# Optimization experiments

Hardware: AMD Instinct MI355X
Metric: run time of the kernel (lower is better)

## Reference

```python
import jax, jax.numpy as jnp
import numpy as np

B, T, C_EMB, C_HEAD = 4, 4096, 1024, 64

def setup_inputs() -> dict:
    key = jax.random.key(0)
    kx, kk, kq, kv = jax.random.split(key, 4)
    x = jax.random.normal(kx, (B, T, C_EMB), dtype=jnp.float32)
    # nn.Linear(C_EMB, C_HEAD, bias=False); store as (in, out) so projection is x @ W
    Wk = jax.random.normal(kk, (C_EMB, C_HEAD), dtype=jnp.float32) * 0.02
    Wq = jax.random.normal(kq, (C_EMB, C_HEAD), dtype=jnp.float32) * 0.02
    Wv = jax.random.normal(kv, (C_EMB, C_HEAD), dtype=jnp.float32) * 0.02
    return {"x": x, "Wk": Wk, "Wq": Wq, "Wv": Wv}

def reference(x, Wk, Wq, Wv):
    k = x @ Wk  # [B,T,Ch]
    q = x @ Wq
    v = x @ Wv
    scale = C_HEAD ** -0.5
    weights = jnp.einsum('bqc,bkc->bqk', q, k) * scale  # [B,T,T]
    causal = jnp.tril(jnp.ones((T, T), dtype=bool))
    weights = jnp.where(causal, weights, -jnp.inf)
    # NOTE: original uses F.softmax(dim=1), i.e. over the QUERY (row) axis -> axis=-2
    weights = jax.nn.softmax(weights, axis=-2)
    # dropout_rate=0.0 (eval) -> identity
    return jnp.einsum('bqk,bkc->bqc', weights, v)
```

## Files before the change

### kernel.cpp

```cpp
#include <hip/hip_runtime.h>
#include <math.h>

#define BB 4
#define TT 4096
#define CE 1024
#define CH 64
#define SCALE2 0.18033688011112042f
#define NQT 64
#define NZ 4

typedef unsigned short ushort_t;
typedef __attribute__((ext_vector_type(8))) short bf16x8;
typedef __attribute__((ext_vector_type(8))) unsigned short u16x8;
typedef __attribute__((ext_vector_type(4))) float f32x4;

__device__ __forceinline__ unsigned short f2bf(float f) {
    unsigned int x = __builtin_bit_cast(unsigned int, f);
    unsigned int r = x + 0x7fffu + ((x >> 16) & 1u);
    return (unsigned short)(r >> 16);
}
__device__ __forceinline__ float bf2f(unsigned short u) {
    unsigned int x = ((unsigned int)u) << 16;
    return __builtin_bit_cast(float, x);
}

__device__ __forceinline__ void stage_tile(const ushort_t* __restrict__ src,
                                           ushort_t (*dst)[68], int tg)
{
#pragma unroll
    for (int i = 0; i < 2; ++i) {
        const int idx = i * 256 + tg;
        const int row = idx >> 3, c0 = (idx & 7) * 8;
        u16x8 v = *(const u16x8*)(src + (long)idx * 8);
        union { u16x8 v; uint2 q[2]; } uu; uu.v = v;
        *(uint2*)&dst[row][c0]     = uu.q[0];
        *(uint2*)&dst[row][c0 + 4] = uu.q[1];
    }
}

__device__ __forceinline__ void stage_tile512(const ushort_t* __restrict__ src,
                                              ushort_t (*dst)[68], int tid)
{
    const int row = tid >> 3, c0 = (tid & 7) * 8;
    u16x8 v = *(const u16x8*)(src + (long)tid * 8);
    union { u16x8 v; uint2 q[2]; } uu; uu.v = v;
    *(uint2*)&dst[row][c0]     = uu.q[0];
    *(uint2*)&dst[row][c0 + 4] = uu.q[1];
}

__device__ __forceinline__ bf16x8 frag68(const ushort_t* p) {
    union { bf16x8 v; uint2 q[2]; } uu;
    uu.q[0] = *(const uint2*)p;
    uu.q[1] = *(const uint2*)(p + 4);
    return uu.v;
}

__global__ __launch_bounds__(256)
void wt_build(const float* __restrict__ Wk, const float* __restrict__ Wq,
              const float* __restrict__ Wv, ushort_t* __restrict__ wt2)
{
    const int m = blockIdx.x, kt = blockIdx.y;
    const float* __restrict__ W = (m == 0) ? Wk : (m == 1 ? Wq : Wv);
    const int k0 = kt * 64;
    __shared__ float lds[64][65];
    const int cc = threadIdx.x & 63, g = threadIdx.x >> 6;
#pragma unroll
    for (int i = 0; i < 16; ++i) {
        const int r = g * 16 + i;
        lds[r][cc] = W[(k0 + r) * CH + cc];
    }
    __syncthreads();
    const int k = k0 + cc;
#pragma unroll
    for (int i = 0; i < 16; ++i) {
        const int c = g * 16 + i;
        wt2[((long)(k >> 5) * 192 + (m * 64 + c)) * 32 + (k & 31)] = f2bf(lds[cc][c]);
    }
}

__global__ __launch_bounds__(512)
void proj_mfma(const float* __restrict__ x, const ushort_t* __restrict__ wt2,
               ushort_t* __restrict__ qb, ushort_t* __restrict__ kb, ushort_t* __restrict__ vb)
{
    const int tid = threadIdx.x;
    const int w = tid >> 6, l = tid & 63, lg = l >> 4, lr = l & 15;
    const int wr = w >> 2, wc = w & 3;
    const long t0 = (long)blockIdx.x * 32;

    __shared__ ushort_t As[32][68];
    __shared__ ushort_t Bs[192][68];

    f32x4 acc[3];
#pragma unroll
    for (int nf = 0; nf < 3; ++nf) acc[nf] = (f32x4){0.f, 0.f, 0.f, 0.f};

    const int arow = tid >> 4, acol = (tid & 15) * 4;
    const float* __restrict__ xsrc = x + (t0 + arow) * CE + acol;

    int bc[3], bh[3], bk[3];
#pragma unroll
    for (int i = 0; i < 3; ++i) {
        const int idx = i * 512 + tid;
        const int h = idx >= 768;
        const int j = idx - h * 768;
        bc[i] = j >> 2; bh[i] = h; bk[i] = (j & 3) * 8;
    }

    float4 a4 = *(const float4*)(xsrc);
    u16x8 bv[3];
#pragma unroll
    for (int i = 0; i < 3; ++i)
        bv[i] = *(const u16x8*)(wt2 + ((long)(bh[i]) * 192 + bc[i]) * 32 + bk[i]);

    for (int step = 0; step < 16; ++step) {
        {
            uint2 pk;
            pk.x = (unsigned)f2bf(a4.x) | ((unsigned)f2bf(a4.y) << 16);
            pk.y = (unsigned)f2bf(a4.z) | ((unsigned)f2bf(a4.w) << 16);
            *(uint2*)&As[arow][acol] = pk;
#pragma unroll
            for (int i = 0; i < 3; ++i) {
                union { u16x8 v; uint2 q[2]; } uu; uu.v = bv[i];
                ushort_t* d = &Bs[bc[i]][bh[i] * 32 + bk[i]];
                *(uint2*)d = uu.q[0];
                *(uint2*)(d + 4) = uu.q[1];
            }
        }
        __syncthreads();
        if (step < 15) {
            const int k0n = (step + 1) * 64;
            a4 = *(const float4*)(xsrc + k0n);
            const int ktn = k0n >> 5;
#pragma unroll
            for (int i = 0; i < 3; ++i)
                bv[i] = *(const u16x8*)(wt2 + ((long)(ktn + bh[i]) * 192 + bc[i]) * 32 + bk[i]);
        }
#pragma unroll
        for (int h = 0; h < 2; ++h) {
            bf16x8 af = frag68(&As[wr * 16 + lr][h * 32 + lg * 8]);
#pragma unroll
            for (int nf = 0; nf < 3; ++nf) {
                bf16x8 bf = frag68(&Bs[wc * 48 + nf * 16 + lr][h * 32 + lg * 8]);
                acc[nf] = __builtin_amdgcn_mfma_f32_16x16x32_bf16(af, bf, acc[nf], 0, 0, 0);
            }
        }
        __syncthreads();
    }

    ushort_t* Os = &Bs[0][0];
#pragma unroll
    for (int nf = 0; nf < 3; ++nf)
#pragma unroll
        for (int r = 0; r < 4; ++r)
            Os[(wr * 16 + lg * 4 + r) * 200 + wc * 48 + nf * 16 + lr] = f2bf(acc[nf][r]);
    __syncthreads();
    if (tid < 256) {
        const int row = tid >> 3, c0 = (tid & 7) * 8;
#pragma unroll
        for (int m = 0; m < 3; ++m) {
            u16x8 ov = *(const u16x8*)&Os[row * 200 + m * 64 + c0];
            ushort_t* __restrict__ outp = (m == 0) ? kb : (m == 1 ? qb : vb);
            *(u16x8*)(outp + (t0 + row) * CH + c0) = ov;
        }
    }
}

__global__ __launch_bounds__(512)
void colstats_mfma(const ushort_t* __restrict__ qb, const ushort_t* __restrict__ kb,
                   float* __restrict__ pl)
{
    const int b = blockIdx.x, p = blockIdx.y, z = blockIdx.z;
    const int tid = threadIdx.x;
    const int w = tid >> 6, l = tid & 63, lg = l >> 4, lr = l & 15;
    const int wg = w >> 2, wc = w & 3, tg = tid & 255;
    const long baseT = (long)b * TT;
    const long NTT = (long)BB * TT;

    __shared__ ushort_t Ks[64][68], Qs[2][64][68];
    __shared__ float redc[4][64][5];

    for (int pass = 0; pass < 2; ++pass) {
        const int kt = pass ? (63 - p) : p;
        stage_tile512(kb + (baseT + (long)kt * 64) * CH, Ks, tid);
        __syncthreads();
        bf16x8 ka0 = frag68(&Ks[wc * 16 + lr][lg * 8]);
        bf16x8 ka1 = frag68(&Ks[wc * 16 + lr][32 + lg * 8]);

        float l_r[4] = {0.f, 0.f, 0.f, 0.f};

        const int j0 = kt + ((z - kt) & (NZ - 1));
        const int n0 = (j0 < NQT) ? ((NQT - 1 - j0) >> 3) + 1 : 0;
        for (int i = 0; i < n0; ++i) {
            const int j = j0 + 4 * wg + 8 * i;
            const bool act = (j < NQT);
            if (act) stage_tile(qb + (baseT + (long)j * 64) * CH, Qs[wg], tg);
            __syncthreads();
            if (act) {
                const bool diag = (j == kt);
#pragma unroll
                for (int qf = 0; qf < 4; ++qf) {
                    bf16x8 b0 = frag68(&Qs[wg][qf * 16 + lr][lg * 8]);
                    bf16x8 b1 = frag68(&Qs[wg][qf * 16 + lr][32 + lg * 8]);
                    f32x4 s = {0.f, 0.f, 0.f, 0.f};
                    s = __builtin_amdgcn_mfma_f32_16x16x32_bf16(ka0, b0, s, 0, 0, 0);
                    s = __builtin_amdgcn_mfma_f32_16x16x32_bf16(ka1, b1, s, 0, 0, 0);
#pragma unroll
                    for (int r = 0; r < 4; ++r) {
                        float ev = exp2f(s[r] * SCALE2);
                        if (diag && (qf * 16 + lr) < (wc * 16 + lg * 4 + r)) ev = 0.f;
                        l_r[r] += ev;
                    }
                }
            }
            __syncthreads();
        }
        if (wg == 1) {
#pragma unroll
            for (int r = 0; r < 4; ++r) redc[wc][l][r] = l_r[r];
        }
        __syncthreads();
        if (wg == 0) {
#pragma unroll
            for (int r = 0; r < 4; ++r) {
                float lv = l_r[r] + redc[wc][l][r];
                for (int d = 1; d < 16; d <<= 1) lv += __shfl_xor(lv, d);
                if (lr == 0) {
                    const long k = (long)kt * 64 + wc * 16 + lg * 4 + r;
                    pl[(long)z * NTT + baseT + k] = lv;
                }
            }
        }
        __syncthreads();
    }
}

__global__ __launch_bounds__(256)
void vt_scale(const ushort_t* __restrict__ vb, const float* __restrict__ pl,
              ushort_t* __restrict__ vtb2)
{
    const int b = blockIdx.x;
    const int jt = blockIdx.y;
    const long t0 = (long)jt * 64;
    const int tid = threadIdx.x;
    __shared__ ushort_t lds[64][72];
    const long baseT = (long)b * TT;
    const long NTT = (long)BB * TT;
#pragma unroll
    for (int i = 0; i < 2; ++i) {
        const int t = i * 32 + (tid >> 3);
        const int c0 = (tid & 7) * 8;
        u16x8 v = *(const u16x8*)(vb + (baseT + t0 + t) * CH + c0);
        const long idx = baseT + t0 + t;
        float ls = pl[idx];
#pragma unroll
        for (int zz = 1; zz < NZ; ++zz) ls += pl[zz * NTT + idx];
        const float sc = 1.f / ls;
#pragma unroll
        for (int j = 0; j < 8; ++j) lds[c0 + j][t] = f2bf(bf2f(v[j]) * sc);
    }
    __syncthreads();
    ushort_t* __restrict__ dst = vtb2 + ((long)(b * 64 + jt)) * (64 * 64);
#pragma unroll
    for (int i = 0; i < 2; ++i) {
        const int c = i * 32 + (tid >> 3);
        const int tt0 = (tid & 7) * 8;
        u16x8 ov = *(const u16x8*)&lds[c][tt0];
        *(u16x8*)(dst + (long)c * 64 + tt0) = ov;
    }
}

__global__ __launch_bounds__(512)
void pv_mfma(const ushort_t* __restrict__ qb, const ushort_t* __restrict__ kb,
             const ushort_t* __restrict__ vtb2, float* __restrict__ pout)
{
    const int b = blockIdx.x, p = blockIdx.y, z = blockIdx.z;
    const int tid = threadIdx.x;
    const int w = tid >> 6, l = tid & 63, lg = l >> 4, lr = l & 15;
    const int wg = w >> 2, wc = w & 3, tg = tid & 255;
    const long baseT = (long)b * TT;
    const long NTT = (long)BB * TT;

    __shared__ ushort_t Qs[64][68], Ks[2][64][68], Vs[2][64][68], Ps[2][64][68];
    __shared__ float redp[4][64][17];

    for (int pass = 0; pass < 2; ++pass) {
        const int qt = pass ? (63 - p) : p;
        stage_tile512(qb + (baseT + (long)qt * 64) * CH, Qs, tid);
        __syncthreads();
        bf16x8 qf_[4][2];
#pragma unroll
        for (int qf = 0; qf < 4; ++qf) {
            qf_[qf][0] = frag68(&Qs[qf * 16 + lr][lg * 8]);
            qf_[qf][1] = frag68(&Qs[qf * 16 + lr][32 + lg * 8]);
        }
        f32x4 o[4];
#pragma unroll
        for (int qf = 0; qf < 4; ++qf) o[qf] = (f32x4){0.f, 0.f, 0.f, 0.f};

        const int n0 = (qt >= z) ? ((qt - z) >> 3) + 1 : 0;
        for (int i = 0; i < n0; ++i) {
            const int j = z + 4 * wg + 8 * i;
            const bool act = (j <= qt);
            if (act) {
                stage_tile(kb + (baseT + (long)j * 64) * CH, Ks[wg], tg);
                stage_tile(vtb2 + ((long)(b * 64 + j)) * (64 * 64), Vs[wg], tg);
            }
            __syncthreads();
            bf16x8 va0, va1;
            if (act) {
                bf16x8 ka0 = frag68(&Ks[wg][wc * 16 + lr][lg * 8]);
                bf16x8 ka1 = frag68(&Ks[wg][wc * 16 + lr][32 + lg * 8]);
                va0 = frag68(&Vs[wg][wc * 16 + lr][lg * 8]);
                va1 = frag68(&Vs[wg][wc * 16 + lr][32 + lg * 8]);
                const bool diag = (j == qt);
#pragma unroll
                for (int qf = 0; qf < 4; ++qf) {
                    f32x4 s = {0.f, 0.f, 0.f, 0.f};
                    s = __builtin_amdgcn_mfma_f32_16x16x32_bf16(ka0, qf_[qf][0], s, 0, 0, 0);
                    s = __builtin_amdgcn_mfma_f32_16x16x32_bf16(ka1, qf_[qf][1], s, 0, 0, 0);
                    unsigned short e[4];
#pragma unroll
                    for (int r = 0; r < 4; ++r) {
                        float ev = exp2f(s[r] * SCALE2);
                        if (diag && (qf * 16 + lr) < (wc * 16 + lg * 4 + r)) ev = 0.f;
                        e[r] = f2bf(ev);
                    }
                    uint2 pk;
                    pk.x = (unsigned)e[0] | ((unsigned)e[1] << 16);
                    pk.y = (unsigned)e[2] | ((unsigned)e[3] << 16);
                    *(uint2*)&Ps[wg][qf * 16 + lr][wc * 16 + lg * 4] = pk;
                }
            }
            __syncthreads();
            if (act) {
#pragma unroll
                for (int qf = 0; qf < 4; ++qf) {
                    bf16x8 p0 = frag68(&Ps[wg][qf * 16 + lr][lg * 8]);
                    bf16x8 p1 = frag68(&Ps[wg][qf * 16 + lr][32 + lg * 8]);
                    o[qf] = __builtin_amdgcn_mfma_f32_16x16x32_bf16(va0, p0, o[qf], 0, 0, 0);
                    o[qf] = __builtin_amdgcn_mfma_f32_16x16x32_bf16(va1, p1, o[qf], 0, 0, 0);
                }
            }
        }
        if (wg == 1) {
#pragma unroll
            for (int qf = 0; qf < 4; ++qf)
#pragma unroll
                for (int r = 0; r < 4; ++r) redp[wc][l][qf * 4 + r] = o[qf][r];
        }
        __syncthreads();
        if (wg == 0) {
            float* pz = pout + ((long)z * NTT + baseT + (long)qt * 64) * CH;
#pragma unroll
            for (int qf = 0; qf < 4; ++qf) {
                f32x4 ov = o[qf];
#pragma unroll
                for (int r = 0; r < 4; ++r) ov[r] += redp[wc][l][qf * 4 + r];
                *(f32x4*)(pz + (long)(qf * 16 + lr) * CH + wc * 16 + lg * 4) = ov;
            }
        }
        __syncthreads();
    }
}

__global__ __launch_bounds__(256)
void finalize_out(const float* __restrict__ pout, float* __restrict__ out)
{
    const long i = (long)blockIdx.x * 256 + threadIdx.x;
    const long n4 = (long)BB * TT * CH / 4;
    float4 r = reinterpret_cast<const float4*>(pout)[i];
#pragma unroll
    for (int zz = 1; zz < NZ; ++zz) {
        float4 a = reinterpret_cast<const float4*>(pout)[zz * n4 + i];
        r.x += a.x; r.y += a.y; r.z += a.z; r.w += a.w;
    }
    reinterpret_cast<float4*>(out)[i] = r;
}

extern "C" void kernel_launch(void* const* d_in, const int* in_sizes, int n_in,
                              void* d_out, int out_size, void* d_ws, size_t ws_size,
                              hipStream_t stream)
{
    const float* x  = (const float*)d_in[0];
    const float* Wk = (const float*)d_in[1];
    const float* Wq = (const float*)d_in[2];
    const float* Wv = (const float*)d_in[3];
    float* out = (float*)d_out;

    const size_t NT = (size_t)BB * TT;
    ushort_t* qb   = (ushort_t*)d_ws;
    ushort_t* kb   = qb + NT * CH;
    ushort_t* vb   = kb + NT * CH;
    ushort_t* vtb2 = vb + NT * CH;
    ushort_t* wt2  = vtb2 + NT * CH;
    float* pl   = (float*)(wt2 + 192 * CE);
    float* pout = pl + NZ * NT;

    hipLaunchKernelGGL(wt_build, dim3(3, 16), dim3(256), 0, stream,
                       Wk, Wq, Wv, wt2);
    hipLaunchKernelGGL(proj_mfma, dim3(NT / 32), dim3(512), 0, stream,
                       x, wt2, qb, kb, vb);
    hipLaunchKernelGGL(colstats_mfma, dim3(BB, NQT / 2, NZ), dim3(512), 0, stream,
                       qb, kb, pl);
    hipLaunchKernelGGL(vt_scale, dim3(BB, TT / 64), dim3(256), 0, stream,
                       vb, pl, vtb2);
    hipLaunchKernelGGL(pv_mfma, dim3(BB, NQT / 2, NZ), dim3(512), 0, stream,
                       qb, kb, vtb2, pout);
    hipLaunchKernelGGL(finalize_out, dim3(NT * CH / 4 / 256), dim3(256), 0, stream,
                       pout, out);
}
```

Measured before the change: 75.89 us.

## Prefetch Q/K/V tiles into registers and fold column normalisation into PV

The colstats and pv kernels now load the next tile into registers while the current tile is computed, a software prefetch that hides global-load latency behind the MFMA work. The projection kernel writes V directly in the transposed tile layout. The vt_scale pass is replaced by a small kernel that computes per-key inverse column sums, and that scale is applied to the exponentials inside pv_mfma. This removes one read and one write of V, at the cost of extra registers and a per-tile float4 load of the inverse sums.

```diff
diff --git a/kernel.cpp b/kernel.cpp
--- a/kernel.cpp
+++ b/kernel.cpp
@@ -24,20 +24,22 @@
     return __builtin_bit_cast(float, x);
 }
 
-__device__ __forceinline__ void stage_tile(const ushort_t* __restrict__ src,
-                                           ushort_t (*dst)[68], int tg)
+__device__ __forceinline__ void tile_load2(const ushort_t* __restrict__ src, int tg, u16x8* r)
+{
+    r[0] = *(const u16x8*)(src + (long)tg * 8);
+    r[1] = *(const u16x8*)(src + (long)(256 + tg) * 8);
+}
+__device__ __forceinline__ void tile_store2(ushort_t (*dst)[68], int tg, const u16x8* r)
 {
 #pragma unroll
     for (int i = 0; i < 2; ++i) {
         const int idx = i * 256 + tg;
         const int row = idx >> 3, c0 = (idx & 7) * 8;
-        u16x8 v = *(const u16x8*)(src + (long)idx * 8);
-        union { u16x8 v; uint2 q[2]; } uu; uu.v = v;
+        union { u16x8 v; uint2 q[2]; } uu; uu.v = r[i];
         *(uint2*)&dst[row][c0]     = uu.q[0];
         *(uint2*)&dst[row][c0 + 4] = uu.q[1];
     }
 }
-
 __device__ __forceinline__ void stage_tile512(const ushort_t* __restrict__ src,
                                               ushort_t (*dst)[68], int tid)
 {
@@ -80,7 +82,7 @@
 
 __global__ __launch_bounds__(512)
 void proj_mfma(const float* __restrict__ x, const ushort_t* __restrict__ wt2,
-               ushort_t* __restrict__ qb, ushort_t* __restrict__ kb, ushort_t* __restrict__ vb)
+               ushort_t* __restrict__ qb, ushort_t* __restrict__ kb, ushort_t* __restrict__ vtb2)
 {
     const int tid = threadIdx.x;
     const int w = tid >> 6, l = tid & 63, lg = l >> 4, lr = l & 15;
@@ -157,11 +159,17 @@
     if (tid < 256) {
         const int row = tid >> 3, c0 = (tid & 7) * 8;
 #pragma unroll
-        for (int m = 0; m < 3; ++m) {
+        for (int m = 0; m < 2; ++m) {
             u16x8 ov = *(const u16x8*)&Os[row * 200 + m * 64 + c0];
-            ushort_t* __restrict__ outp = (m == 0) ? kb : (m == 1 ? qb : vb);
+            ushort_t* __restrict__ outp = (m == 0) ? kb : qb;
             *(u16x8*)(outp + (t0 + row) * CH + c0) = ov;
         }
+        const int c = tid >> 2, ii = tid & 3;
+        u16x8 tv;
+#pragma unroll
+        for (int k = 0; k < 8; ++k) tv[k] = Os[(ii * 8 + k) * 200 + 128 + c];
+        const int bI = (int)(t0 / TT), jt = (int)((t0 % TT) >> 6), toff = (int)(t0 & 63);
+        *(u16x8*)(vtb2 + (((long)(bI * 64 + jt) * 64 + c) * 64) + toff + ii * 8) = tv;
     }
 }
 
@@ -182,19 +190,27 @@
     for (int pass = 0; pass < 2; ++pass) {
         const int kt = pass ? (63 - p) : p;
         stage_tile512(kb + (baseT + (long)kt * 64) * CH, Ks, tid);
+
+        float l_r[4] = {0.f, 0.f, 0.f, 0.f};
+        const int j0 = kt + ((z - kt) & (NZ - 1));
+        const int n0 = (j0 < NQT) ? ((NQT - 1 - j0) >> 3) + 1 : 0;
+
+        u16x8 qreg[2];
+        {
+            const int j = j0 + 4 * wg;
+            if (j < NQT) tile_load2(qb + (baseT + (long)j * 64) * CH, tg, qreg);
+        }
         __syncthreads();
         bf16x8 ka0 = frag68(&Ks[wc * 16 + lr][lg * 8]);
         bf16x8 ka1 = frag68(&Ks[wc * 16 + lr][32 + lg * 8]);
 
-        float l_r[4] = {0.f, 0.f, 0.f, 0.f};
-
-        const int j0 = kt + ((z - kt) & (NZ - 1));
-        const int n0 = (j0 < NQT) ? ((NQT - 1 - j0) >> 3) + 1 : 0;
         for (int i = 0; i < n0; ++i) {
             const int j = j0 + 4 * wg + 8 * i;
             const bool act = (j < NQT);
-            if (act) stage_tile(qb + (baseT + (long)j * 64) * CH, Qs[wg], tg);
+            if (act) tile_store2(Qs[wg], tg, qreg);
             __syncthreads();
+            const int jn = j + 8;
+            if (jn < NQT) tile_load2(qb + (baseT + (long)jn * 64) * CH, tg, qreg);
             if (act) {
                 const bool diag = (j == kt);
 #pragma unroll
@@ -235,43 +251,20 @@
 }
 
 __global__ __launch_bounds__(256)
-void vt_scale(const ushort_t* __restrict__ vb, const float* __restrict__ pl,
-              ushort_t* __restrict__ vtb2)
-{
-    const int b = blockIdx.x;
-    const int jt = blockIdx.y;
-    const long t0 = (long)jt * 64;
-    const int tid = threadIdx.x;
-    __shared__ ushort_t lds[64][72];
-    const long baseT = (long)b * TT;
+void linv_kernel(const float* __restrict__ pl, float* __restrict__ linv)
+{
+    const long i = (long)blockIdx.x * 256 + threadIdx.x;
     const long NTT = (long)BB * TT;
-#pragma unroll
-    for (int i = 0; i < 2; ++i) {
-        const int t = i * 32 + (tid >> 3);
-        const int c0 = (tid & 7) * 8;
-        u16x8 v = *(const u16x8*)(vb + (baseT + t0 + t) * CH + c0);
-        const long idx = baseT + t0 + t;
-        float ls = pl[idx];
-#pragma unroll
-        for (int zz = 1; zz < NZ; ++zz) ls += pl[zz * NTT + idx];
-        const float sc = 1.f / ls;
-#pragma unroll
-        for (int j = 0; j < 8; ++j) lds[c0 + j][t] = f2bf(bf2f(v[j]) * sc);
-    }
-    __syncthreads();
-    ushort_t* __restrict__ dst = vtb2 + ((long)(b * 64 + jt)) * (64 * 64);
-#pragma unroll
-    for (int i = 0; i < 2; ++i) {
-        const int c = i * 32 + (tid >> 3);
-        const int tt0 = (tid & 7) * 8;
-        u16x8 ov = *(const u16x8*)&lds[c][tt0];
-        *(u16x8*)(dst + (long)c * 64 + tt0) = ov;
-    }
+    float s = pl[i];
+#pragma unroll
+    for (int zz = 1; zz < NZ; ++zz) s += pl[zz * NTT + i];
+    linv[i] = 1.f / s;
 }
 
 __global__ __launch_bounds__(512)
 void pv_mfma(const ushort_t* __restrict__ qb, const ushort_t* __restrict__ kb,
-             const ushort_t* __restrict__ vtb2, float* __restrict__ pout)
+             const ushort_t* __restrict__ vtb2, const float* __restrict__ linv,
+             float* __restrict__ pout)
 {
     const int b = blockIdx.x, p = blockIdx.y, z = blockIdx.z;
     const int tid = threadIdx.x;
@@ -286,6 +279,16 @@
     for (int pass = 0; pass < 2; ++pass) {
         const int qt = pass ? (63 - p) : p;
         stage_tile512(qb + (baseT + (long)qt * 64) * CH, Qs, tid);
+
+        const int n0 = (qt >= z) ? ((qt - z) >> 3) + 1 : 0;
+        u16x8 kreg[2], vreg[2];
+        {
+            const int j = z + 4 * wg;
+            if (j <= qt) {
+                tile_load2(kb + (baseT + (long)j * 64) * CH, tg, kreg);
+                tile_load2(vtb2 + ((long)(b * 64 + j)) * 4096, tg, vreg);
+            }
+        }
         __syncthreads();
         bf16x8 qf_[4][2];
 #pragma unroll
@@ -297,21 +300,27 @@
 #pragma unroll
         for (int qf = 0; qf < 4; ++qf) o[qf] = (f32x4){0.f, 0.f, 0.f, 0.f};
 
-        const int n0 = (qt >= z) ? ((qt - z) >> 3) + 1 : 0;
         for (int i = 0; i < n0; ++i) {
             const int j = z + 4 * wg + 8 * i;
             const bool act = (j <= qt);
             if (act) {
-                stage_tile(kb + (baseT + (long)j * 64) * CH, Ks[wg], tg);
-                stage_tile(vtb2 + ((long)(b * 64 + j)) * (64 * 64), Vs[wg], tg);
+                tile_store2(Ks[wg], tg, kreg);
+                tile_store2(Vs[wg], tg, vreg);
             }
             __syncthreads();
+            const int jn = j + 8;
+            if (jn <= qt) {
+                tile_load2(kb + (baseT + (long)jn * 64) * CH, tg, kreg);
+                tile_load2(vtb2 + ((long)(b * 64 + jn)) * 4096, tg, vreg);
+            }
             bf16x8 va0, va1;
             if (act) {
                 bf16x8 ka0 = frag68(&Ks[wg][wc * 16 + lr][lg * 8]);
                 bf16x8 ka1 = frag68(&Ks[wg][wc * 16 + lr][32 + lg * 8]);
                 va0 = frag68(&Vs[wg][wc * 16 + lr][lg * 8]);
                 va1 = frag68(&Vs[wg][wc * 16 + lr][32 + lg * 8]);
+                float4 lv4 = *(const float4*)(linv + baseT + (long)j * 64 + wc * 16 + lg * 4);
+                const float lvr[4] = {lv4.x, lv4.y, lv4.z, lv4.w};
                 const bool diag = (j == qt);
 #pragma unroll
                 for (int qf = 0; qf < 4; ++qf) {
@@ -321,7 +330,7 @@
                     unsigned short e[4];
 #pragma unroll
                     for (int r = 0; r < 4; ++r) {
-                        float ev = exp2f(s[r] * SCALE2);
+                        float ev = exp2f(s[r] * SCALE2) * lvr[r];
                         if (diag && (qf * 16 + lr) < (wc * 16 + lg * 4 + r)) ev = 0.f;
                         e[r] = f2bf(ev);
                     }
@@ -390,22 +399,22 @@
     const size_t NT = (size_t)BB * TT;
     ushort_t* qb   = (ushort_t*)d_ws;
     ushort_t* kb   = qb + NT * CH;
-    ushort_t* vb   = kb + NT * CH;
-    ushort_t* vtb2 = vb + NT * CH;
+    ushort_t* vtb2 = kb + NT * CH;
     ushort_t* wt2  = vtb2 + NT * CH;
     float* pl   = (float*)(wt2 + 192 * CE);
-    float* pout = pl + NZ * NT;
+    float* linv = pl + NZ * NT;
+    float* pout = linv + NT;
 
     hipLaunchKernelGGL(wt_build, dim3(3, 16), dim3(256), 0, stream,
                        Wk, Wq, Wv, wt2);
     hipLaunchKernelGGL(proj_mfma, dim3(NT / 32), dim3(512), 0, stream,
-                       x, wt2, qb, kb, vb);
+                       x, wt2, qb, kb, vtb2);
     hipLaunchKernelGGL(colstats_mfma, dim3(BB, NQT / 2, NZ), dim3(512), 0, stream,
                        qb, kb, pl);
-    hipLaunchKernelGGL(vt_scale, dim3(BB, TT / 64), dim3(256), 0, stream,
-                       vb, pl, vtb2);
+    hipLaunchKernelGGL(linv_kernel, dim3(NT / 256), dim3(256), 0, stream,
+                       pl, linv);
     hipLaunchKernelGGL(pv_mfma, dim3(BB, NQT / 2, NZ), dim3(512), 0, stream,
-                       qb, kb, vtb2, pout);
+                       qb, kb, vtb2, linv, pout);
     hipLaunchKernelGGL(finalize_out, dim3(NT * CH / 4 / 256), dim3(256), 0, stream,
                        pout, out);
 }
```

New measurement: 83.20 us. +9.6%, slower.

## Prefetch tiles into registers and launch one tile per block in attention kernels

Applied to the files above, without the earlier changes.

Both colstats and pv kernels now load the next Q (or K/V) tile into registers while the current tile is being computed, then write it to LDS at the top of the next iteration. This hides global-memory latency behind MFMA work. The paired two-pass scheme per block is dropped in favour of one tile per block with twice as many blocks, and pv_mfma reverses tile order so the heaviest tiles are scheduled first. LDS use is reduced by aliasing the reduction buffer onto Ks and reusing Qs as one wave group's P buffer, which may raise occupancy but also raises register pressure.

```diff
diff --git a/kernel.cpp b/kernel.cpp
--- a/kernel.cpp
+++ b/kernel.cpp
@@ -24,20 +24,22 @@
     return __builtin_bit_cast(float, x);
 }
 
-__device__ __forceinline__ void stage_tile(const ushort_t* __restrict__ src,
-                                           ushort_t (*dst)[68], int tg)
+__device__ __forceinline__ void tile_load2(const ushort_t* __restrict__ src, int tg, u16x8* r)
+{
+    r[0] = *(const u16x8*)(src + (long)tg * 8);
+    r[1] = *(const u16x8*)(src + (long)(256 + tg) * 8);
+}
+__device__ __forceinline__ void tile_store2(ushort_t (*dst)[68], int tg, const u16x8* r)
 {
 #pragma unroll
     for (int i = 0; i < 2; ++i) {
         const int idx = i * 256 + tg;
         const int row = idx >> 3, c0 = (idx & 7) * 8;
-        u16x8 v = *(const u16x8*)(src + (long)idx * 8);
-        union { u16x8 v; uint2 q[2]; } uu; uu.v = v;
+        union { u16x8 v; uint2 q[2]; } uu; uu.v = r[i];
         *(uint2*)&dst[row][c0]     = uu.q[0];
         *(uint2*)&dst[row][c0 + 4] = uu.q[1];
     }
 }
-
 __device__ __forceinline__ void stage_tile512(const ushort_t* __restrict__ src,
                                               ushort_t (*dst)[68], int tid)
 {
@@ -169,7 +171,7 @@
 void colstats_mfma(const ushort_t* __restrict__ qb, const ushort_t* __restrict__ kb,
                    float* __restrict__ pl)
 {
-    const int b = blockIdx.x, p = blockIdx.y, z = blockIdx.z;
+    const int b = blockIdx.x, kt = blockIdx.y, z = blockIdx.z;
     const int tid = threadIdx.x;
     const int w = tid >> 6, l = tid & 63, lg = l >> 4, lr = l & 15;
     const int wg = w >> 2, wc = w & 3, tg = tid & 255;
@@ -179,58 +181,62 @@
     __shared__ ushort_t Ks[64][68], Qs[2][64][68];
     __shared__ float redc[4][64][5];
 
-    for (int pass = 0; pass < 2; ++pass) {
-        const int kt = pass ? (63 - p) : p;
-        stage_tile512(kb + (baseT + (long)kt * 64) * CH, Ks, tid);
-        __syncthreads();
-        bf16x8 ka0 = frag68(&Ks[wc * 16 + lr][lg * 8]);
-        bf16x8 ka1 = frag68(&Ks[wc * 16 + lr][32 + lg * 8]);
-
-        float l_r[4] = {0.f, 0.f, 0.f, 0.f};
-
-        const int j0 = kt + ((z - kt) & (NZ - 1));
-        const int n0 = (j0 < NQT) ? ((NQT - 1 - j0) >> 3) + 1 : 0;
-        for (int i = 0; i < n0; ++i) {
-            const int j = j0 + 4 * wg + 8 * i;
-            const bool act = (j < NQT);
-            if (act) stage_tile(qb + (baseT + (long)j * 64) * CH, Qs[wg], tg);
-            __syncthreads();
-            if (act) {
-                const bool diag = (j == kt);
-#pragma unroll
-                for (int qf = 0; qf < 4; ++qf) {
-                    bf16x8 b0 = frag68(&Qs[wg][qf * 16 + lr][lg * 8]);
-                    bf16x8 b1 = frag68(&Qs[wg][qf * 16 + lr][32 + lg * 8]);
-                    f32x4 s = {0.f, 0.f, 0.f, 0.f};
-                    s = __builtin_amdgcn_mfma_f32_16x16x32_bf16(ka0, b0, s, 0, 0, 0);
-                    s = __builtin_amdgcn_mfma_f32_16x16x32_bf16(ka1, b1, s, 0, 0, 0);
-#pragma unroll
-                    for (int r = 0; r < 4; ++r) {
-                        float ev = exp2f(s[r] * SCALE2);
-                        if (diag && (qf * 16 + lr) < (wc * 16 + lg * 4 + r)) ev = 0.f;
-                        l_r[r] += ev;
-                    }
+    stage_tile512(kb + (baseT + (long)kt * 64) * CH, Ks, tid);
+
+    float l_r[4] = {0.f, 0.f, 0.f, 0.f};
+    const int j0 = kt + ((z - kt) & (NZ - 1));
+    const int n0 = (j0 < NQT) ? ((NQT - 1 - j0) >> 3) + 1 : 0;
+
+    u16x8 qreg[2];
+    {
+        const int j = j0 + 4 * wg;
+        if (j < NQT) tile_load2(qb + (baseT + (long)j * 64) * CH, tg, qreg);
+    }
+    __syncthreads();
+    bf16x8 ka0 = frag68(&Ks[wc * 16 + lr][lg * 8]);
+    bf16x8 ka1 = frag68(&Ks[wc * 16 + lr][32 + lg * 8]);
+
+    for (int i = 0; i < n0; ++i) {
+        const int j = j0 + 4 * wg + 8 * i;
+        const bool act = (j < NQT);
+        if (act) tile_store2(Qs[wg], tg, qreg);
+        __syncthreads();
+        const int jn = j + 8;
+        if (jn < NQT) tile_load2(qb + (baseT + (long)jn * 64) * CH, tg, qreg);
+        if (act) {
+            const bool diag = (j == kt);
+#pragma unroll
+            for (int qf = 0; qf < 4; ++qf) {
+                bf16x8 b0 = frag68(&Qs[wg][qf * 16 + lr][lg * 8]);
+                bf16x8 b1 = frag68(&Qs[wg][qf * 16 + lr][32 + lg * 8]);
+                f32x4 s = {0.f, 0.f, 0.f, 0.f};
+                s = __builtin_amdgcn_mfma_f32_16x16x32_bf16(ka0, b0, s, 0, 0, 0);
+                s = __builtin_amdgcn_mfma_f32_16x16x32_bf16(ka1, b1, s, 0, 0, 0);
+#pragma unroll
+                for (int r = 0; r < 4; ++r) {
+                    float ev = exp2f(s[r] * SCALE2);
+                    if (diag && (qf * 16 + lr) < (wc * 16 + lg * 4 + r)) ev = 0.f;
+                    l_r[r] += ev;
                 }
             }
-            __syncthreads();
-        }
-        if (wg == 1) {
-#pragma unroll
-            for (int r = 0; r < 4; ++r) redc[wc][l][r] = l_r[r];
-        }
-        __syncthreads();
-        if (wg == 0) {
-#pragma unroll
-            for (int r = 0; r < 4; ++r) {
-                float lv = l_r[r] + redc[wc][l][r];
-                for (int d = 1; d < 16; d <<= 1) lv += __shfl_xor(lv, d);
-                if (lr == 0) {
-                    const long k = (long)kt * 64 + wc * 16 + lg * 4 + r;
-                    pl[(long)z * NTT + baseT + k] = lv;
-                }
-            }
-        }
-        __syncthreads();
+        }
+        __syncthreads();
+    }
+    if (wg == 1) {
+#pragma unroll
+        for (int r = 0; r < 4; ++r) redc[wc][l][r] = l_r[r];
+    }
+    __syncthreads();
+    if (wg == 0) {
+#pragma unroll
+        for (int r = 0; r < 4; ++r) {
+            float lv = l_r[r] + redc[wc][l][r];
+            for (int d = 1; d < 16; d <<= 1) lv += __shfl_xor(lv, d);
+            if (lr == 0) {
+                const long k = (long)kt * 64 + wc * 16 + lg * 4 + r;
+                pl[(long)z * NTT + baseT + k] = lv;
+            }
+        }
     }
 }
 
@@ -273,93 +279,110 @@
 void pv_mfma(const ushort_t* __restrict__ qb, const ushort_t* __restrict__ kb,
              const ushort_t* __restrict__ vtb2, float* __restrict__ pout)
 {
-    const int b = blockIdx.x, p = blockIdx.y, z = blockIdx.z;
+    const int b = blockIdx.x, z = blockIdx.z;
+    const int qt = 63 - blockIdx.y;
     const int tid = threadIdx.x;
     const int w = tid >> 6, l = tid & 63, lg = l >> 4, lr = l & 15;
     const int wg = w >> 2, wc = w & 3, tg = tid & 255;
     const long baseT = (long)b * TT;
     const long NTT = (long)BB * TT;
 
-    __shared__ ushort_t Qs[64][68], Ks[2][64][68], Vs[2][64][68], Ps[2][64][68];
-    __shared__ float redp[4][64][17];
-
-    for (int pass = 0; pass < 2; ++pass) {
-        const int qt = pass ? (63 - p) : p;
-        stage_tile512(qb + (baseT + (long)qt * 64) * CH, Qs, tid);
-        __syncthreads();
-        bf16x8 qf_[4][2];
+    __shared__ ushort_t Qs[64][68];
+    __shared__ ushort_t Ks[2][64][68];
+    __shared__ ushort_t Vs[2][64][68];
+    __shared__ ushort_t Ps1[64][68];
+    float (*redp)[64][17] = (float (*)[64][17])&Ks[0][0][0];
+
+    stage_tile512(qb + (baseT + (long)qt * 64) * CH, Qs, tid);
+
+    const int n0 = (qt >= z) ? ((qt - z) >> 3) + 1 : 0;
+    u16x8 kreg[2], vreg[2];
+    {
+        const int j = z + 4 * wg;
+        if (j <= qt) {
+            tile_load2(kb + (baseT + (long)j * 64) * CH, tg, kreg);
+            tile_load2(vtb2 + ((long)(b * 64 + j)) * 4096, tg, vreg);
+        }
+    }
+    __syncthreads();
+    bf16x8 qf_[4][2];
+#pragma unroll
+    for (int qf = 0; qf < 4; ++qf) {
+        qf_[qf][0] = frag68(&Qs[qf * 16 + lr][lg * 8]);
+        qf_[qf][1] = frag68(&Qs[qf * 16 + lr][32 + lg * 8]);
+    }
+    f32x4 o[4];
+#pragma unroll
+    for (int qf = 0; qf < 4; ++qf) o[qf] = (f32x4){0.f, 0.f, 0.f, 0.f};
+
+    ushort_t (*Pbuf)[68] = (wg == 0) ? Qs : Ps1;
+
+    for (int i = 0; i < n0; ++i) {
+        const int j = z + 4 * wg + 8 * i;
+        const bool act = (j <= qt);
+        if (act) {
+            tile_store2(Ks[wg], tg, kreg);
+            tile_store2(Vs[wg], tg, vreg);
+        }
+        __syncthreads();
+        const int jn = j + 8;
+        if (jn <= qt) {
+            tile_load2(kb + (baseT + (long)jn * 64) * CH, tg, kreg);
+            tile_load2(vtb2 + ((long)(b * 64 + jn)) * 4096, tg, vreg);
+        }
+        bf16x8 va0, va1;
+        if (act) {
+            bf16x8 ka0 = frag68(&Ks[wg][wc * 16 + lr][lg * 8]);
+            bf16x8 ka1 = frag68(&Ks[wg][wc * 16 + lr][32 + lg * 8]);
+            va0 = frag68(&Vs[wg][wc * 16 + lr][lg * 8]);
+            va1 = frag68(&Vs[wg][wc * 16 + lr][32 + lg * 8]);
+            const bool diag = (j == qt);
+#pragma unroll
+            for (int qf = 0; qf < 4; ++qf) {
+                f32x4 s = {0.f, 0.f, 0.f, 0.f};
+                s = __builtin_amdgcn_mfma_f32_16x16x32_bf16(ka0, qf_[qf][0], s, 0, 0, 0);
+                s = __builtin_amdgcn_mfma_f32_16x16x32_bf16(ka1, qf_[qf][1], s, 0, 0, 0);
+                unsigned short e[4];
+#pragma unroll
+                for (int r = 0; r < 4; ++r) {
+                    float ev = exp2f(s[r] * SCALE2);
+                    if (diag && (qf * 16 + lr) < (wc * 16 + lg * 4 + r)) ev = 0.f;
+                    e[r] = f2bf(ev);
+                }
+                uint2 pk;
+                pk.x = (unsigned)e[0] | ((unsigned)e[1] << 16);
+                pk.y = (unsigned)e[2] | ((unsigned)e[3] << 16);
+                *(uint2*)&Pbuf[qf * 16 + lr][wc * 16 + lg * 4] = pk;
+            }
+        }
+        __syncthreads();
+        if (act) {
+#pragma unroll
+            for (int qf = 0; qf < 4; ++qf) {
+                bf16x8 p0 = frag68(&Pbuf[qf * 16 + lr][lg * 8]);
+                bf16x8 p1 = frag68(&Pbuf[qf * 16 + lr][32 + lg * 8]);
+                o[qf] = __builtin_amdgcn_mfma_f32_16x16x32_bf16(va0, p0, o[qf], 0, 0, 0);
+                o[qf] = __builtin_amdgcn_mfma_f32_16x16x32_bf16(va1, p1, o[qf], 0, 0, 0);
+            }
+        }
+        __syncthreads();
+    }
+    if (wg == 1) {
+#pragma unroll
+        for (int qf = 0; qf < 4; ++qf)
+#pragma unroll
+            for (int r = 0; r < 4; ++r) redp[wc][l][qf * 4 + r] = o[qf][r];
+    }
+    __syncthreads();
+    if (wg == 0) {
+        float* pz = pout + ((long)z * NTT + baseT + (long)qt * 64) * CH;
 #pragma unroll
         for (int qf = 0; qf < 4; ++qf) {
-            qf_[qf][0] = frag68(&Qs[qf * 16 + lr][lg * 8]);
-            qf_[qf][1] = frag68(&Qs[qf * 16 + lr][32 + lg * 8]);
-        }
-        f32x4 o[4];
-#pragma unroll
-        for (int qf = 0; qf < 4; ++qf) o[qf] = (f32x4){0.f, 0.f, 0.f, 0.f};
-
-        const int n0 = (qt >= z) ? ((qt - z) >> 3) + 1 : 0;
-        for (int i = 0; i < n0; ++i) {
-            const int j = z + 4 * wg + 8 * i;
-            const bool act = (j <= qt);
-            if (act) {
-                stage_tile(kb + (baseT + (long)j * 64) * CH, Ks[wg], tg);
-                stage_tile(vtb2 + ((long)(b * 64 + j)) * (64 * 64), Vs[wg], tg);
-            }
-            __syncthreads();
-            bf16x8 va0, va1;
-            if (act) {
-                bf16x8 ka0 = frag68(&Ks[wg][wc * 16 + lr][lg * 8]);
-                bf16x8 ka1 = frag68(&Ks[wg][wc * 16 + lr][32 + lg * 8]);
-                va0 = frag68(&Vs[wg][wc * 16 + lr][lg * 8]);
-                va1 = frag68(&Vs[wg][wc * 16 + lr][32 + lg * 8]);
-                const bool diag = (j == qt);
-#pragma unroll
-                for (int qf = 0; qf < 4; ++qf) {
-                    f32x4 s = {0.f, 0.f, 0.f, 0.f};
-                    s = __builtin_amdgcn_mfma_f32_16x16x32_bf16(ka0, qf_[qf][0], s, 0, 0, 0);
-                    s = __builtin_amdgcn_mfma_f32_16x16x32_bf16(ka1, qf_[qf][1], s, 0, 0, 0);
-                    unsigned short e[4];
-#pragma unroll
-                    for (int r = 0; r < 4; ++r) {
-                        float ev = exp2f(s[r] * SCALE2);
-                        if (diag && (qf * 16 + lr) < (wc * 16 + lg * 4 + r)) ev = 0.f;
-                        e[r] = f2bf(ev);
-                    }
-                    uint2 pk;
-                    pk.x = (unsigned)e[0] | ((unsigned)e[1] << 16);
-                    pk.y = (unsigned)e[2] | ((unsigned)e[3] << 16);
-                    *(uint2*)&Ps[wg][qf * 16 + lr][wc * 16 + lg * 4] = pk;
-                }
-            }
-            __syncthreads();
-            if (act) {
-#pragma unroll
-                for (int qf = 0; qf < 4; ++qf) {
-                    bf16x8 p0 = frag68(&Ps[wg][qf * 16 + lr][lg * 8]);
-                    bf16x8 p1 = frag68(&Ps[wg][qf * 16 + lr][32 + lg * 8]);
-                    o[qf] = __builtin_amdgcn_mfma_f32_16x16x32_bf16(va0, p0, o[qf], 0, 0, 0);
-                    o[qf] = __builtin_amdgcn_mfma_f32_16x16x32_bf16(va1, p1, o[qf], 0, 0, 0);
-                }
-            }
-        }
-        if (wg == 1) {
-#pragma unroll
-            for (int qf = 0; qf < 4; ++qf)
-#pragma unroll
-                for (int r = 0; r < 4; ++r) redp[wc][l][qf * 4 + r] = o[qf][r];
-        }
-        __syncthreads();
-        if (wg == 0) {
-            float* pz = pout + ((long)z * NTT + baseT + (long)qt * 64) * CH;
-#pragma unroll
-            for (int qf = 0; qf < 4; ++qf) {
-                f32x4 ov = o[qf];
-#pragma unroll
-                for (int r = 0; r < 4; ++r) ov[r] += redp[wc][l][qf * 4 + r];
-                *(f32x4*)(pz + (long)(qf * 16 + lr) * CH + wc * 16 + lg * 4) = ov;
-            }
-        }
-        __syncthreads();
+            f32x4 ov = o[qf];
+#pragma unroll
+            for (int r = 0; r < 4; ++r) ov[r] += redp[wc][l][qf * 4 + r];
+            *(f32x4*)(pz + (long)(qf * 16 + lr) * CH + wc * 16 + lg * 4) = ov;
+        }
     }
 }
 
@@ -400,11 +423,11 @@
                        Wk, Wq, Wv, wt2);
     hipLaunchKernelGGL(proj_mfma, dim3(NT / 32), dim3(512), 0, stream,
                        x, wt2, qb, kb, vb);
-    hipLaunchKernelGGL(colstats_mfma, dim3(BB, NQT / 2, NZ), dim3(512), 0, stream,
+    hipLaunchKernelGGL(colstats_mfma, dim3(BB, NQT, NZ), dim3(512), 0, stream,
                        qb, kb, pl);
     hipLaunchKernelGGL(vt_scale, dim3(BB, TT / 64), dim3(256), 0, stream,
                        vb, pl, vtb2);
-    hipLaunchKernelGGL(pv_mfma, dim3(BB, NQT / 2, NZ), dim3(512), 0, stream,
+    hipLaunchKernelGGL(pv_mfma, dim3(BB, NQT, NZ), dim3(512), 0, stream,
                        qb, kb, vtb2, pout);
     hipLaunchKernelGGL(finalize_out, dim3(NT * CH / 4 / 256), dim3(256), 0, stream,
                        pout, out);
```

Result: slower. 86.10 us (+13.5%).
